# Optimization experiments

Hardware: AMD Instinct MI355X
Metric: run time of the kernel (lower is better)

The kernel has to match this reference:

```python
import jax, jax.numpy as jnp
import numpy as np


def _layernorm(x, g, b, eps=1e-6):
    mu = jnp.mean(x, -1, keepdims=True)
    var = jnp.var(x, -1, keepdims=True)
    return (x - mu) * jax.lax.rsqrt(var + eps) * g + b


def _rope_interleave(x, cos, sin):
    # de-interleave pairs (x0,x1),(x2,x3),... -> [evens | odds]  (matches
    # torch view(..., d//2, 2).transpose(-1,-2).reshape(..., d))
    x = jnp.concatenate([x[..., 0::2], x[..., 1::2]], axis=-1)
    d = x.shape[-1]
    x1, x2 = x[..., : d // 2], x[..., d // 2 :]
    rot = jnp.concatenate([-x2, x1], axis=-1)
    return x * cos + rot * sin


def setup_inputs() -> dict:
    key = jax.random.key(0)
    k = jax.random.split(key, 6)
    T, H, D, R, HID, QLR, K = 2048, 32, 128, 64, 4096, 1536, 256
    hidden_states = jax.random.normal(k[0], (1, T, HID), jnp.float32)
    q_latent = jax.random.normal(k[1], (1, T, QLR), jnp.float32)
    wq_b = jax.random.normal(k[2], (QLR, H * D), jnp.float32) * 0.02
    wk = jax.random.normal(k[3], (HID, D), jnp.float32) * 0.02
    w_proj = jax.random.normal(k[4], (HID, H), jnp.float32) * 0.02
    k_gamma = jnp.ones((D,), jnp.float32)
    k_beta = jnp.zeros((D,), jnp.float32)
    # real rotary cos/sin tables for the 64-dim rope slice
    pos = jnp.arange(T, dtype=jnp.float32)
    inv_freq = 1.0 / (10000.0 ** (jnp.arange(0, R, 2, dtype=jnp.float32) / R))
    freqs = jnp.outer(pos, inv_freq)
    emb = jnp.concatenate([freqs, freqs], axis=-1)  # [T, R]
    cos, sin = jnp.cos(emb), jnp.sin(emb)
    ks = jnp.zeros((T,), jnp.int32)
    ke = jnp.arange(1, T + 1, dtype=jnp.int32)  # causal: keys [0, t]
    return dict(hidden_states=hidden_states, q_latent=q_latent, ks=ks, ke=ke,
                cos=cos, sin=sin, wq_b=wq_b, wk=wk, k_gamma=k_gamma,
                k_beta=k_beta, w_proj=w_proj, index_topk=K)


def reference(hidden_states, q_latent, ks, ke, cos, sin, wq_b, wk,
              k_gamma, k_beta, w_proj, index_topk):
    T = hidden_states.shape[1]
    H = w_proj.shape[1]
    D = wk.shape[1]
    R = cos.shape[-1]
    weight_scale = (D ** -0.5) * (H ** -0.5)

    q = (q_latent[0] @ wq_b).reshape(T, H, D)              # [T,H,D]
    k = _layernorm(hidden_states[0] @ wk, k_gamma, k_beta)  # [T,D]
    w = hidden_states[0] @ w_proj                           # [T,H]

    q_pe = _rope_interleave(q[..., :R], cos[:, None, :], sin[:, None, :])
    k_pe = _rope_interleave(k[..., :R], cos, sin)
    q = jnp.concatenate([q_pe, q[..., R:]], axis=-1)
    k = jnp.concatenate([k_pe, k[..., R:]], axis=-1)

    # lightning-indexer score: I[t,s] = sum_h w[t,h] * relu(q[t,h] . k[s])
    scores = jnp.einsum('thd,sd->ths', q, k)                # [T,H,S]
    scores = jnp.einsum('ths,th->ts', jax.nn.relu(scores), w) * weight_scale

    j = jnp.arange(T)
    mask = (j[None, :] >= ks[:, None]) & (j[None, :] < ke[:, None])
    scores = jnp.where(mask, scores, -1e30)
    values, idx = jax.lax.top_k(scores, index_topk)
    return idx.reshape(1, T, 1, index_topk), values
```

## Files before the change

### kernel.cpp

```cpp
#include <hip/hip_runtime.h>
#include <cstdint>

typedef unsigned short u16;
typedef unsigned int   u32;
typedef unsigned long long u64;

typedef short bf16x8 __attribute__((ext_vector_type(8)));
typedef float f32x4  __attribute__((ext_vector_type(4)));
typedef u16   u16x8  __attribute__((ext_vector_type(8)));

__device__ __forceinline__ u16 f2b(float f){
  u32 u = __float_as_uint(f);
  u += 0x7FFFu + ((u >> 16) & 1u);
  return (u16)(u >> 16);
}
__device__ __forceinline__ float b2f(u16 h){ return __uint_as_float(((u32)h) << 16); }
__device__ __forceinline__ u32 fkey(float f){
  u32 u = __float_as_uint(f);
  return u ^ ((u & 0x80000000u) ? 0xFFFFFFFFu : 0x80000000u);
}
__device__ __forceinline__ float unkey(u32 k){
  u32 u = (k & 0x80000000u) ? (k ^ 0x80000000u) : ~k;
  return __uint_as_float(u);
}
__device__ __forceinline__ void gload16(const void* g, void* l){
  __builtin_amdgcn_global_load_lds(
      reinterpret_cast<const __attribute__((address_space(1))) char*>(reinterpret_cast<uintptr_t>(g)),
      reinterpret_cast<__attribute__((address_space(3))) char*>(reinterpret_cast<uintptr_t>(l)),
      16, 0, 0);
}

__global__ __launch_bounds__(256) void k_init(const int* __restrict__ ke, int* __restrict__ list){
  __shared__ int km[64];
  int tid = threadIdx.x;
  if (tid < 64){
    int m = 0;
    for (int j = 0; j < 32; j++) m = max(m, ke[tid * 32 + j]);
    km[tid] = m;
  }
  __syncthreads();
  if (tid < 8){
    int x = tid, n = 0;
    for (int j0 = 0; j0 < 8; j0++){
      int tb = j0 * 8 + x;
      int kmax = km[tb];
      for (int sb = 0; sb < 16; sb++){
        if (sb * 128 < kmax){
          list[n * 8 + x] = tb * 32 + sb * 2 + 0; n++;
          list[n * 8 + x] = tb * 32 + sb * 2 + 1; n++;
        }
      }
    }
    for (; n < 256; n++) list[n * 8 + x] = -1;
  }
}

__global__ __launch_bounds__(256) void k_cvt(const float* __restrict__ in, u16* __restrict__ out, int n8){
  int i = blockIdx.x * 256 + threadIdx.x;
  if (i >= n8) return;
  const float4* p = (const float4*)in + (size_t)i * 2;
  float4 a = p[0], b = p[1];
  u16x8 v;
  v[0]=f2b(a.x); v[1]=f2b(a.y); v[2]=f2b(a.z); v[3]=f2b(a.w);
  v[4]=f2b(b.x); v[5]=f2b(b.y); v[6]=f2b(b.z); v[7]=f2b(b.w);
  *((u16x8*)out + i) = v;
}

__global__ __launch_bounds__(256) void k_tcvt(const float* __restrict__ in, u16* __restrict__ out, int R, int C){
  __shared__ float tile[32][33];
  int c0 = blockIdx.x * 32, r0 = blockIdx.y * 32;
  int tx = threadIdx.x & 31, ty = threadIdx.x >> 5;
  for (int i = 0; i < 4; i++){
    int r = ty * 4 + i;
    tile[r][tx] = in[(size_t)(r0 + r) * C + c0 + tx];
  }
  __syncthreads();
  for (int i = 0; i < 4; i++){
    int c = ty * 4 + i;
    out[(size_t)(c0 + c) * R + r0 + tx] = f2b(tile[tx][c]);
  }
}

__global__ __launch_bounds__(256) void k_wct(const float* __restrict__ wk, const float* __restrict__ wp, u16* __restrict__ out){
  __shared__ float tile[32][33];
  int c0 = blockIdx.x * 32, i0 = blockIdx.y * 32;
  int tx = threadIdx.x & 31, ty = threadIdx.x >> 5;
  for (int j = 0; j < 4; j++){
    int i = i0 + ty * 4 + j;
    int c = c0 + tx;
    float v = 0.f;
    if (c < 128) v = wk[(size_t)i * 128 + c];
    else if (c < 160) v = wp[(size_t)i * 32 + (c - 128)];
    tile[ty * 4 + j][tx] = v;
  }
  __syncthreads();
  for (int j = 0; j < 4; j++){
    int c = c0 + ty * 4 + j;
    out[(size_t)c * 4096 + i0 + tx] = f2b(tile[tx][ty * 4 + j]);
  }
}

__global__ __launch_bounds__(256) void k_gemm_kw(const float* __restrict__ A, const u16* __restrict__ B, float* __restrict__ Cp){
  const int Kd = 4096, NC = 192;
  __shared__ float As[128 * 64];
  __shared__ u16 Bs[64 * 64];
  int lin = blockIdx.x;
  int xcd = lin & 7, idx = lin >> 3;
  int nb = idx % 3, pz = idx / 3;
  int p = xcd + 8 * pz;
  int m0 = (p & 15) * 128;
  int kt0 = (p >> 4) * 512;
  int n0 = nb * 64;
  float* C = Cp + (size_t)(p >> 4) * 2048 * NC;
  int tid = threadIdx.x, lane = tid & 63, wid = tid >> 6;
  int wm = wid * 32;
  f32x4 acc[2][4] = {};
  for (int kt = kt0; kt < kt0 + 512; kt += 64){
    for (int c = tid; c < 2048; c += 256){
      int row = c >> 4, slot = (c & 15) ^ (row & 7);
      gload16(A + (size_t)(m0 + row) * Kd + kt + slot * 4, (float*)As + (size_t)c * 4);
    }
    for (int c = tid; c < 512; c += 256){
      int row = c >> 3, slot = (c & 7) ^ (row & 7);
      gload16(B + (size_t)(n0 + row) * Kd + kt + slot * 8, (u16*)Bs + (size_t)c * 8);
    }
    __syncthreads();
    for (int kk = 0; kk < 2; kk++){
      bf16x8 af[2], bfr[4];
      for (int i = 0; i < 2; i++){
        int row = wm + i * 16 + (lane & 15);
        int c0 = kk * 8 + (lane >> 4) * 2;
        f32x4 lo = *(const f32x4*)&As[row * 64 + ((c0)     ^ (row & 7)) * 4];
        f32x4 hi = *(const f32x4*)&As[row * 64 + ((c0 + 1) ^ (row & 7)) * 4];
        bf16x8 t;
        t[0]=(short)f2b(lo[0]); t[1]=(short)f2b(lo[1]); t[2]=(short)f2b(lo[2]); t[3]=(short)f2b(lo[3]);
        t[4]=(short)f2b(hi[0]); t[5]=(short)f2b(hi[1]); t[6]=(short)f2b(hi[2]); t[7]=(short)f2b(hi[3]);
        af[i] = t;
      }
      for (int j = 0; j < 4; j++){
        int row = j * 16 + (lane & 15);
        int slot = (kk * 4 + (lane >> 4)) ^ (row & 7);
        bfr[j] = *(const bf16x8*)&Bs[row * 64 + slot * 8];
      }
      for (int i = 0; i < 2; i++)
        for (int j = 0; j < 4; j++)
          acc[i][j] = __builtin_amdgcn_mfma_f32_16x16x32_bf16(af[i], bfr[j], acc[i][j], 0, 0, 0);
    }
    __syncthreads();
  }
  for (int i = 0; i < 2; i++)
    for (int j = 0; j < 4; j++){
      int row = m0 + wm + i * 16 + ((lane >> 4) * 4);
      int col = n0 + j * 16 + (lane & 15);
      for (int r = 0; r < 4; r++)
        C[(size_t)(row + r) * NC + col] = acc[i][j][r];
    }
}

__global__ __launch_bounds__(256) void k_lnrope(const float* __restrict__ kwp, const float* __restrict__ gamma,
                                                const float* __restrict__ beta, const float* __restrict__ cosp,
                                                const float* __restrict__ sinp, u16* __restrict__ krot,
                                                float* __restrict__ wfin){
  const size_t ZS = (size_t)2048 * 192;
  int row = blockIdx.x * 4 + (threadIdx.x >> 6);
  int lane = threadIdx.x & 63;
  const float* x = kwp + (size_t)row * 192;
  float2 v = {0.f, 0.f};
  for (int z = 0; z < 8; z++){
    float2 p = *(const float2*)&x[z * ZS + lane * 2];
    v.x += p.x; v.y += p.y;
  }
  float s = v.x + v.y, ss = v.x * v.x + v.y * v.y;
  for (int o = 32; o; o >>= 1){ s += __shfl_xor(s, o); ss += __shfl_xor(ss, o); }
  float mu = s * (1.f / 128.f);
  float var = ss * (1.f / 128.f) - mu * mu;
  float rs = rsqrtf(var + 1e-6f);
  float y0 = (v.x - mu) * rs * gamma[lane * 2]     + beta[lane * 2];
  float y1 = (v.y - mu) * rs * gamma[lane * 2 + 1] + beta[lane * 2 + 1];
  u16* out = krot + (size_t)row * 128;
  if (lane < 32){
    float c = cosp[(size_t)row * 64 + lane], sn = sinp[(size_t)row * 64 + lane];
    out[lane]      = f2b(y0 * c - y1 * sn);
    out[lane + 32] = f2b(y1 * c + y0 * sn);
    float wsum = 0.f;
    for (int z = 0; z < 8; z++) wsum += x[z * ZS + 128 + lane];
    wfin[(size_t)row * 32 + lane] = wsum;
  } else {
    out[lane * 2]     = f2b(y0);
    out[lane * 2 + 1] = f2b(y1);
  }
}

__global__ __launch_bounds__(256) void k_gemm_q(const u16* __restrict__ A, const u16* __restrict__ B,
                                                const float* __restrict__ cosp, const float* __restrict__ sinp,
                                                u16* __restrict__ C){
  const int N = 4096, Kd = 1536;
  __shared__ u16 As[128 * 64];
  __shared__ u16 Bs[128 * 64];
  int linb = blockIdx.x;
  int xcd = linb & 7, loc = linb >> 3;
  int n0 = (xcd * 4 + (loc >> 4)) * 128;
  int m0 = (loc & 15) * 128;
  int tid = threadIdx.x, lane = tid & 63, wid = tid >> 6;
  int wm = (wid >> 1) * 64, wn = (wid & 1) * 64;
  f32x4 acc[4][4] = {};
  for (int kt = 0; kt < Kd; kt += 64){
    for (int c = tid; c < 1024; c += 256){
      int row = c >> 3, slot = (c & 7) ^ (row & 7);
      gload16(A + (size_t)(m0 + row) * Kd + kt + slot * 8, (u16*)As + (size_t)c * 8);
      gload16(B + (size_t)(n0 + row) * Kd + kt + slot * 8, (u16*)Bs + (size_t)c * 8);
    }
    __syncthreads();
    for (int kk = 0; kk < 2; kk++){
      bf16x8 af[4], bfr[4];
      for (int i = 0; i < 4; i++){
        int rowa = wm + i * 16 + (lane & 15);
        int rowb = wn + i * 16 + (lane & 15);
        int sa = (kk * 4 + (lane >> 4)) ^ (rowa & 7);
        int sbx = (kk * 4 + (lane >> 4)) ^ (rowb & 7);
        af[i]  = *(const bf16x8*)&As[rowa * 64 + sa * 8];
        bfr[i] = *(const bf16x8*)&Bs[rowb * 64 + sbx * 8];
      }
      for (int i = 0; i < 4; i++)
        for (int j = 0; j < 4; j++)
          acc[i][j] = __builtin_amdgcn_mfma_f32_16x16x32_bf16(af[i], bfr[j], acc[i][j], 0, 0, 0);
    }
    __syncthreads();
  }
  if (wn == 0){
    int l = lane & 15;
    int base = lane & 48;
    int sl = base + ((2 * l) & 15);
    for (int i = 0; i < 4; i++){
      int rowb = m0 + wm + i * 16 + ((lane >> 4) * 4);
      f32x4 ne[4];
      for (int j = 0; j < 4; j++){
        int jj = j & 1;
        for (int r = 0; r < 4; r++){
          float eA = __shfl(acc[i][2 * jj][r],     sl);
          float eB = __shfl(acc[i][2 * jj + 1][r], sl);
          float oA = __shfl(acc[i][2 * jj][r],     sl + 1);
          float oB = __shfl(acc[i][2 * jj + 1][r], sl + 1);
          float e = (l >= 8) ? eB : eA;
          float o = (l >= 8) ? oB : oA;
          int row = rowb + r;
          int d = j * 16 + l;
          float c = cosp[(size_t)row * 64 + d];
          float s = sinp[(size_t)row * 64 + d];
          ne[j][r] = (j < 2) ? (e * c - o * s) : (o * c + e * s);
        }
      }
      for (int j = 0; j < 4; j++) acc[i][j] = ne[j];
    }
  }
  for (int i = 0; i < 4; i++)
    for (int j = 0; j < 4; j++){
      int row = m0 + wm + i * 16 + ((lane >> 4) * 4);
      int col = n0 + wn + j * 16 + (lane & 15);
      for (int r = 0; r < 4; r++)
        C[(size_t)(row + r) * N + col] = f2b(acc[i][j][r]);
    }
}

__global__ __launch_bounds__(256, 4) void k_scores(const u16* __restrict__ q, const u16* __restrict__ krot,
                                                   const float* __restrict__ wfin, const int* __restrict__ list,
                                                   float* __restrict__ S0, float* __restrict__ S1){
  __shared__ u16 Bs[128 * 128];
  __shared__ float Ws[16][32];
  int e = list[blockIdx.x];
  if (e < 0) return;
  int tb = e >> 5, sb = (e >> 1) & 15, hgrp = e & 1;
  int t0 = tb * 32, s0 = sb * 128;
  int tid = threadIdx.x, lane = tid & 63, wid = tid >> 6;
  int wr = wid >> 1, wc = wid & 1;

  for (int c = tid; c < 2048; c += 256){
    int row = c >> 4, slot = (c & 15) ^ (row & 7);
    gload16(krot + (size_t)(s0 + row) * 128 + slot * 8, (u16*)Bs + (size_t)c * 8);
  }
  for (int i = tid; i < 512; i += 256){
    int h = i >> 5, r = i & 31;
    Ws[h][r] = wfin[(size_t)(t0 + r) * 32 + hgrp * 16 + h];
  }
  __syncthreads();

  bf16x8 bfr[4][4];
  for (int j = 0; j < 4; j++)
    for (int kc = 0; kc < 4; kc++){
      int row = wc * 64 + j * 16 + (lane & 15);
      int slot = (kc * 4 + (lane >> 4)) ^ (row & 7);
      bfr[j][kc] = *(const bf16x8*)&Bs[row * 128 + slot * 8];
    }

  f32x4 acc[4] = {};
  const u16* qbase = q + ((size_t)t0 + wr * 16 + (lane & 15)) * 4096 + (size_t)hgrp * 16 * 128 + (lane >> 4) * 8;
  int rbase = wr * 16 + ((lane >> 4) * 4);
  for (int h = 0; h < 16; h++){
    bf16x8 af[4];
    for (int kc = 0; kc < 4; kc++)
      af[kc] = *(const bf16x8*)&qbase[h * 128 + kc * 32];
    f32x4 ah[4] = {};
    for (int kc = 0; kc < 4; kc++)
      for (int j = 0; j < 4; j++)
        ah[j] = __builtin_amdgcn_mfma_f32_16x16x32_bf16(af[kc], bfr[j][kc], ah[j], 0, 0, 0);
    for (int r = 0; r < 4; r++){
      float wv = Ws[h][rbase + r];
      for (int j = 0; j < 4; j++)
        acc[j][r] += fmaxf(ah[j][r], 0.f) * wv;
    }
  }
  float* Sp = hgrp ? S1 : S0;
  for (int j = 0; j < 4; j++){
    int col = s0 + wc * 64 + j * 16 + (lane & 15);
    for (int r = 0; r < 4; r++)
      Sp[(size_t)(t0 + rbase + r) * 2048 + col] = acc[j][r];
  }
}

__global__ __launch_bounds__(256) void k_topk(const float* __restrict__ S0, const float* __restrict__ S1,
                                              const int* __restrict__ ktp, const int* __restrict__ ksv,
                                              const int* __restrict__ ke, float* __restrict__ out){
  int t = blockIdx.x;
  int T = gridDim.x;
  const float* r0 = S0 + (size_t)t * 2048;
  const float* r1 = S1 + (size_t)t * 2048;
  __shared__ u32 keys[2048];
  __shared__ u32 hist[256];
  __shared__ u32 ssum[256];
  __shared__ u32 sb, srem;
  __shared__ u32 wtot[8];
  __shared__ int selIdx[256];
  __shared__ u32 baseGt, baseTie;
  __shared__ u64 skey[256];
  int tid = threadIdx.x;
  int K = ktp[0]; if (K > 256) K = 256;
  int ket = ke[t]; if (ket < 0) ket = 0; if (ket > 2048) ket = 2048;
  int kst = ksv[t]; if (kst < 0) kst = 0;
  int limit = (ket + 255) & ~255;
  if (limit < 256) limit = 256;
  if (limit > 2048) limit = 2048;
  const u32 kneg = fkey(-1e30f);
  const float scale = 0.015625f;
  for (int i4 = tid; i4 < (limit >> 2); i4 += 256){
    int base = i4 * 4;
    float4 a = ((const float4*)r0)[i4];
    float4 b = ((const float4*)r1)[i4];
    float v0 = (a.x + b.x) * scale, v1 = (a.y + b.y) * scale;
    float v2 = (a.z + b.z) * scale, v3 = (a.w + b.w) * scale;
    keys[base + 0] = (base + 0 >= kst && base + 0 < ket) ? fkey(v0) : kneg;
    keys[base + 1] = (base + 1 >= kst && base + 1 < ket) ? fkey(v1) : kneg;
    keys[base + 2] = (base + 2 >= kst && base + 2 < ket) ? fkey(v2) : kneg;
    keys[base + 3] = (base + 3 >= kst && base + 3 < ket) ? fkey(v3) : kneg;
  }
  __syncthreads();
  if (limit > K){
    u32 prefix = 0, pmask = 0, rem = (u32)K;
    for (int p = 3; p >= 0; p--){
      int sh = p * 8;
      hist[tid] = 0;
      __syncthreads();
      for (int i = tid; i < limit; i += 256){
        u32 u = keys[i];
        if ((u & pmask) == prefix) atomicAdd(&hist[(u >> sh) & 255], 1u);
      }
      __syncthreads();
      ssum[tid] = hist[tid];
      __syncthreads();
      for (int off = 1; off < 256; off <<= 1){
        u32 add = (tid + off < 256) ? ssum[tid + off] : 0u;
        __syncthreads();
        ssum[tid] += add;
        __syncthreads();
      }
      u32 mine = ssum[tid];
      u32 above = (tid == 255) ? 0u : ssum[tid + 1];
      if (mine >= rem && above < rem){ sb = (u32)tid; srem = rem - above; }
      __syncthreads();
      prefix |= (sb << sh);
      pmask |= (255u << sh);
      rem = srem;
      __syncthreads();
    }
    u32 thr = prefix;
    int G = K - (int)rem;
    if (tid == 0){ baseGt = 0; baseTie = 0; }
    __syncthreads();
    int nch = limit >> 8;
    for (int ch = 0; ch < nch; ch++){
      int i = ch * 256 + tid;
      u32 u = keys[i];
      bool gt = (u > thr), tie = (u == thr);
      u64 bg = __ballot(gt), bt = __ballot(tie);
      int lane = tid & 63, w = tid >> 6;
      if (lane == 0){ wtot[w] = (u32)__popcll(bg); wtot[4 + w] = (u32)__popcll(bt); }
      __syncthreads();
      u32 og = baseGt, ot = baseTie;
      for (int ww = 0; ww < w; ww++){ og += wtot[ww]; ot += wtot[4 + ww]; }
      og += (u32)__popcll(bg & ((1ull << lane) - 1ull));
      ot += (u32)__popcll(bt & ((1ull << lane) - 1ull));
      if (gt) selIdx[og] = i;
      else if (tie && ot < rem) selIdx[G + ot] = i;
      __syncthreads();
      if (tid == 0){
        for (int ww = 0; ww < 4; ww++){ baseGt += wtot[ww]; baseTie += wtot[4 + ww]; }
      }
      __syncthreads();
    }
    if (tid < K){
      int si = selIdx[tid];
      u32 u = keys[si];
      skey[tid] = ((u64)(~u) << 32) | (u32)si;
    } else {
      skey[tid] = ~0ull;
    }
  } else {
    if (tid < K) skey[tid] = ((u64)(~keys[tid]) << 32) | (u32)tid;
    else skey[tid] = ~0ull;
  }
  __syncthreads();
  for (int size = 2; size <= 256; size <<= 1){
    for (int stride = size >> 1; stride > 0; stride >>= 1){
      int p = tid ^ stride;
      if (p > tid){
        bool up = ((tid & size) == 0);
        u64 a = skey[tid], b = skey[p];
        if ((a > b) == up){ skey[tid] = b; skey[p] = a; }
      }
      __syncthreads();
    }
  }
  if (tid < K){
    u64 sk = skey[tid];
    int idx = (int)(u32)(sk & 0xFFFFFFFFu);
    float val = unkey(~(u32)(sk >> 32));
    out[(size_t)t * K + tid] = (float)idx;
    out[(size_t)T * K + (size_t)t * K + tid] = val;
  }
}

extern "C" void kernel_launch(void* const* d_in, const int* in_sizes, int n_in,
                              void* d_out, int out_size, void* d_ws, size_t ws_size,
                              hipStream_t stream){
  const float* hs   = (const float*)d_in[0];
  const float* ql   = (const float*)d_in[1];
  const int*   ks   = (const int*)  d_in[2];
  const int*   ke   = (const int*)  d_in[3];
  const float* cosp = (const float*)d_in[4];
  const float* sinp = (const float*)d_in[5];
  const float* wqb  = (const float*)d_in[6];
  const float* wk   = (const float*)d_in[7];
  const float* kg   = (const float*)d_in[8];
  const float* kb   = (const float*)d_in[9];
  const float* wp   = (const float*)d_in[10];
  const int*   ktp  = (const int*)  d_in[11];

  char* w = (char*)d_ws;
  u16* qlb = (u16*)w;  w += (size_t)2048 * 1536 * 2;
  u16* wqT = (u16*)w;  w += (size_t)4096 * 1536 * 2;
  u16* wct = (u16*)w;  w += (size_t)192 * 4096 * 2;
  u16* qb  = (u16*)w;  w += (size_t)2048 * 4096 * 2;
  float* kwp = (float*)w; w += (size_t)8 * 2048 * 192 * 4;
  float* wfin = (float*)w; w += (size_t)2048 * 32 * 4;
  u16* krt = (u16*)w;  w += (size_t)2048 * 128 * 2;
  float* S0 = (float*)w; w += (size_t)2048 * 2048 * 4;
  int* list = (int*)w;  w += 2048 * 4;
  float* S1 = (float*)d_ws;

  hipLaunchKernelGGL(k_init, dim3(1), dim3(256), 0, stream, ke, list);
  hipLaunchKernelGGL(k_cvt, dim3(1536), dim3(256), 0, stream, ql, qlb, 393216);
  hipLaunchKernelGGL(k_tcvt, dim3(128, 48), dim3(256), 0, stream, wqb, wqT, 1536, 4096);
  hipLaunchKernelGGL(k_wct, dim3(6, 128), dim3(256), 0, stream, wk, wp, wct);
  hipLaunchKernelGGL(k_gemm_kw, dim3(384), dim3(256), 0, stream, hs, wct, kwp);
  hipLaunchKernelGGL(k_lnrope, dim3(512), dim3(256), 0, stream, kwp, kg, kb, cosp, sinp, krt, wfin);
  hipLaunchKernelGGL(k_gemm_q, dim3(512), dim3(256), 0, stream, qlb, wqT, cosp, sinp, qb);
  hipLaunchKernelGGL(k_scores, dim3(2048), dim3(256), 0, stream, qb, krt, wfin, list, S0, S1);
  hipLaunchKernelGGL(k_topk, dim3(2048), dim3(256), 0, stream, S0, S1, ktp, ks, ke, (float*)d_out);
}
```

Measured before the change: 158.3 us.

## Merge Q-projection and K/W-projection GEMMs into one horizontally fused launch

```diff
diff --git a/kernel.cpp b/kernel.cpp
--- a/kernel.cpp
+++ b/kernel.cpp
@@ -100,61 +100,134 @@
   }
 }
 
-__global__ __launch_bounds__(256) void k_gemm_kw(const float* __restrict__ A, const u16* __restrict__ B, float* __restrict__ Cp){
-  const int Kd = 4096, NC = 192;
-  __shared__ float As[128 * 64];
-  __shared__ u16 Bs[64 * 64];
-  int lin = blockIdx.x;
-  int xcd = lin & 7, idx = lin >> 3;
-  int nb = idx % 3, pz = idx / 3;
-  int p = xcd + 8 * pz;
-  int m0 = (p & 15) * 128;
-  int kt0 = (p >> 4) * 512;
-  int n0 = nb * 64;
-  float* C = Cp + (size_t)(p >> 4) * 2048 * NC;
+__global__ __launch_bounds__(256) void k_gemm_fused(const u16* __restrict__ Aq, const u16* __restrict__ Bq,
+                                                    const float* __restrict__ cosp, const float* __restrict__ sinp,
+                                                    u16* __restrict__ Cq,
+                                                    const float* __restrict__ Akw, const u16* __restrict__ Bkw,
+                                                    float* __restrict__ Cp){
+  __shared__ char smem[40960];
   int tid = threadIdx.x, lane = tid & 63, wid = tid >> 6;
-  int wm = wid * 32;
-  f32x4 acc[2][4] = {};
-  for (int kt = kt0; kt < kt0 + 512; kt += 64){
-    for (int c = tid; c < 2048; c += 256){
-      int row = c >> 4, slot = (c & 15) ^ (row & 7);
-      gload16(A + (size_t)(m0 + row) * Kd + kt + slot * 4, (float*)As + (size_t)c * 4);
-    }
-    for (int c = tid; c < 512; c += 256){
-      int row = c >> 3, slot = (c & 7) ^ (row & 7);
-      gload16(B + (size_t)(n0 + row) * Kd + kt + slot * 8, (u16*)Bs + (size_t)c * 8);
-    }
-    __syncthreads();
-    for (int kk = 0; kk < 2; kk++){
-      bf16x8 af[2], bfr[4];
-      for (int i = 0; i < 2; i++){
-        int row = wm + i * 16 + (lane & 15);
-        int c0 = kk * 8 + (lane >> 4) * 2;
-        f32x4 lo = *(const f32x4*)&As[row * 64 + ((c0)     ^ (row & 7)) * 4];
-        f32x4 hi = *(const f32x4*)&As[row * 64 + ((c0 + 1) ^ (row & 7)) * 4];
-        bf16x8 t;
-        t[0]=(short)f2b(lo[0]); t[1]=(short)f2b(lo[1]); t[2]=(short)f2b(lo[2]); t[3]=(short)f2b(lo[3]);
-        t[4]=(short)f2b(hi[0]); t[5]=(short)f2b(hi[1]); t[6]=(short)f2b(hi[2]); t[7]=(short)f2b(hi[3]);
-        af[i] = t;
-      }
+  if (blockIdx.x < 512){
+    const int N = 4096, Kd = 1536;
+    u16* As = (u16*)smem;
+    u16* Bs = (u16*)(smem + 16384);
+    int linb = blockIdx.x;
+    int xcd = linb & 7, loc = linb >> 3;
+    int n0 = (xcd * 4 + (loc >> 4)) * 128;
+    int m0 = (loc & 15) * 128;
+    int wm = (wid >> 1) * 64, wn = (wid & 1) * 64;
+    f32x4 acc[4][4] = {};
+    for (int kt = 0; kt < Kd; kt += 64){
+      for (int c = tid; c < 1024; c += 256){
+        int row = c >> 3, slot = (c & 7) ^ (row & 7);
+        gload16(Aq + (size_t)(m0 + row) * Kd + kt + slot * 8, As + (size_t)c * 8);
+        gload16(Bq + (size_t)(n0 + row) * Kd + kt + slot * 8, Bs + (size_t)c * 8);
+      }
+      __syncthreads();
+      for (int kk = 0; kk < 2; kk++){
+        bf16x8 af[4], bfr[4];
+        for (int i = 0; i < 4; i++){
+          int rowa = wm + i * 16 + (lane & 15);
+          int rowb = wn + i * 16 + (lane & 15);
+          int sa = (kk * 4 + (lane >> 4)) ^ (rowa & 7);
+          int sbx = (kk * 4 + (lane >> 4)) ^ (rowb & 7);
+          af[i]  = *(const bf16x8*)&As[rowa * 64 + sa * 8];
+          bfr[i] = *(const bf16x8*)&Bs[rowb * 64 + sbx * 8];
+        }
+        for (int i = 0; i < 4; i++)
+          for (int j = 0; j < 4; j++)
+            acc[i][j] = __builtin_amdgcn_mfma_f32_16x16x32_bf16(af[i], bfr[j], acc[i][j], 0, 0, 0);
+      }
+      __syncthreads();
+    }
+    if (wn == 0){
+      int l = lane & 15;
+      int base = lane & 48;
+      int sl = base + ((2 * l) & 15);
+      for (int i = 0; i < 4; i++){
+        int rowb = m0 + wm + i * 16 + ((lane >> 4) * 4);
+        f32x4 ne[4];
+        for (int j = 0; j < 4; j++){
+          int jj = j & 1;
+          for (int r = 0; r < 4; r++){
+            float eA = __shfl(acc[i][2 * jj][r],     sl);
+            float eB = __shfl(acc[i][2 * jj + 1][r], sl);
+            float oA = __shfl(acc[i][2 * jj][r],     sl + 1);
+            float oB = __shfl(acc[i][2 * jj + 1][r], sl + 1);
+            float e = (l >= 8) ? eB : eA;
+            float o = (l >= 8) ? oB : oA;
+            int row = rowb + r;
+            int d = j * 16 + l;
+            float c = cosp[(size_t)row * 64 + d];
+            float s = sinp[(size_t)row * 64 + d];
+            ne[j][r] = (j < 2) ? (e * c - o * s) : (o * c + e * s);
+          }
+        }
+        for (int j = 0; j < 4; j++) acc[i][j] = ne[j];
+      }
+    }
+    for (int i = 0; i < 4; i++)
       for (int j = 0; j < 4; j++){
-        int row = j * 16 + (lane & 15);
-        int slot = (kk * 4 + (lane >> 4)) ^ (row & 7);
-        bfr[j] = *(const bf16x8*)&Bs[row * 64 + slot * 8];
-      }
-      for (int i = 0; i < 2; i++)
-        for (int j = 0; j < 4; j++)
-          acc[i][j] = __builtin_amdgcn_mfma_f32_16x16x32_bf16(af[i], bfr[j], acc[i][j], 0, 0, 0);
-    }
-    __syncthreads();
-  }
-  for (int i = 0; i < 2; i++)
-    for (int j = 0; j < 4; j++){
-      int row = m0 + wm + i * 16 + ((lane >> 4) * 4);
-      int col = n0 + j * 16 + (lane & 15);
-      for (int r = 0; r < 4; r++)
-        C[(size_t)(row + r) * NC + col] = acc[i][j][r];
-    }
+        int row = m0 + wm + i * 16 + ((lane >> 4) * 4);
+        int col = n0 + wn + j * 16 + (lane & 15);
+        for (int r = 0; r < 4; r++)
+          Cq[(size_t)(row + r) * N + col] = f2b(acc[i][j][r]);
+      }
+  } else {
+    const int Kd = 4096, NC = 192;
+    float* As = (float*)smem;
+    u16* Bs = (u16*)(smem + 32768);
+    int lin = blockIdx.x - 512;
+    int xcd = lin & 7, idx = lin >> 3;
+    int nb = idx % 3, pz = idx / 3;
+    int p = xcd + 8 * pz;
+    int m0 = (p & 15) * 128;
+    int kt0 = (p >> 4) * 512;
+    int n0 = nb * 64;
+    float* C = Cp + (size_t)(p >> 4) * 2048 * NC;
+    int wm = wid * 32;
+    f32x4 acc[2][4] = {};
+    for (int kt = kt0; kt < kt0 + 512; kt += 64){
+      for (int c = tid; c < 2048; c += 256){
+        int row = c >> 4, slot = (c & 15) ^ (row & 7);
+        gload16(Akw + (size_t)(m0 + row) * Kd + kt + slot * 4, As + (size_t)c * 4);
+      }
+      for (int c = tid; c < 512; c += 256){
+        int row = c >> 3, slot = (c & 7) ^ (row & 7);
+        gload16(Bkw + (size_t)(n0 + row) * Kd + kt + slot * 8, Bs + (size_t)c * 8);
+      }
+      __syncthreads();
+      for (int kk = 0; kk < 2; kk++){
+        bf16x8 af[2], bfr[4];
+        for (int i = 0; i < 2; i++){
+          int row = wm + i * 16 + (lane & 15);
+          int c0 = kk * 8 + (lane >> 4) * 2;
+          f32x4 lo = *(const f32x4*)&As[row * 64 + ((c0)     ^ (row & 7)) * 4];
+          f32x4 hi = *(const f32x4*)&As[row * 64 + ((c0 + 1) ^ (row & 7)) * 4];
+          bf16x8 t;
+          t[0]=(short)f2b(lo[0]); t[1]=(short)f2b(lo[1]); t[2]=(short)f2b(lo[2]); t[3]=(short)f2b(lo[3]);
+          t[4]=(short)f2b(hi[0]); t[5]=(short)f2b(hi[1]); t[6]=(short)f2b(hi[2]); t[7]=(short)f2b(hi[3]);
+          af[i] = t;
+        }
+        for (int j = 0; j < 4; j++){
+          int row = j * 16 + (lane & 15);
+          int slot = (kk * 4 + (lane >> 4)) ^ (row & 7);
+          bfr[j] = *(const bf16x8*)&Bs[row * 64 + slot * 8];
+        }
+        for (int i = 0; i < 2; i++)
+          for (int j = 0; j < 4; j++)
+            acc[i][j] = __builtin_amdgcn_mfma_f32_16x16x32_bf16(af[i], bfr[j], acc[i][j], 0, 0, 0);
+      }
+      __syncthreads();
+    }
+    for (int i = 0; i < 2; i++)
+      for (int j = 0; j < 4; j++){
+        int row = m0 + wm + i * 16 + ((lane >> 4) * 4);
+        int col = n0 + j * 16 + (lane & 15);
+        for (int r = 0; r < 4; r++)
+          C[(size_t)(row + r) * NC + col] = acc[i][j][r];
+      }
+  }
 }
 
 __global__ __launch_bounds__(256) void k_lnrope(const float* __restrict__ kwp, const float* __restrict__ gamma,
@@ -189,77 +262,6 @@
     out[lane * 2]     = f2b(y0);
     out[lane * 2 + 1] = f2b(y1);
   }
-}
-
-__global__ __launch_bounds__(256) void k_gemm_q(const u16* __restrict__ A, const u16* __restrict__ B,
-                                                const float* __restrict__ cosp, const float* __restrict__ sinp,
-                                                u16* __restrict__ C){
-  const int N = 4096, Kd = 1536;
-  __shared__ u16 As[128 * 64];
-  __shared__ u16 Bs[128 * 64];
-  int linb = blockIdx.x;
-  int xcd = linb & 7, loc = linb >> 3;
-  int n0 = (xcd * 4 + (loc >> 4)) * 128;
-  int m0 = (loc & 15) * 128;
-  int tid = threadIdx.x, lane = tid & 63, wid = tid >> 6;
-  int wm = (wid >> 1) * 64, wn = (wid & 1) * 64;
-  f32x4 acc[4][4] = {};
-  for (int kt = 0; kt < Kd; kt += 64){
-    for (int c = tid; c < 1024; c += 256){
-      int row = c >> 3, slot = (c & 7) ^ (row & 7);
-      gload16(A + (size_t)(m0 + row) * Kd + kt + slot * 8, (u16*)As + (size_t)c * 8);
-      gload16(B + (size_t)(n0 + row) * Kd + kt + slot * 8, (u16*)Bs + (size_t)c * 8);
-    }
-    __syncthreads();
-    for (int kk = 0; kk < 2; kk++){
-      bf16x8 af[4], bfr[4];
-      for (int i = 0; i < 4; i++){
-        int rowa = wm + i * 16 + (lane & 15);
-        int rowb = wn + i * 16 + (lane & 15);
-        int sa = (kk * 4 + (lane >> 4)) ^ (rowa & 7);
-        int sbx = (kk * 4 + (lane >> 4)) ^ (rowb & 7);
-        af[i]  = *(const bf16x8*)&As[rowa * 64 + sa * 8];
-        bfr[i] = *(const bf16x8*)&Bs[rowb * 64 + sbx * 8];
-      }
-      for (int i = 0; i < 4; i++)
-        for (int j = 0; j < 4; j++)
-          acc[i][j] = __builtin_amdgcn_mfma_f32_16x16x32_bf16(af[i], bfr[j], acc[i][j], 0, 0, 0);
-    }
-    __syncthreads();
-  }
-  if (wn == 0){
-    int l = lane & 15;
-    int base = lane & 48;
-    int sl = base + ((2 * l) & 15);
-    for (int i = 0; i < 4; i++){
-      int rowb = m0 + wm + i * 16 + ((lane >> 4) * 4);
-      f32x4 ne[4];
-      for (int j = 0; j < 4; j++){
-        int jj = j & 1;
-        for (int r = 0; r < 4; r++){
-          float eA = __shfl(acc[i][2 * jj][r],     sl);
-          float eB = __shfl(acc[i][2 * jj + 1][r], sl);
-          float oA = __shfl(acc[i][2 * jj][r],     sl + 1);
-          float oB = __shfl(acc[i][2 * jj + 1][r], sl + 1);
-          float e = (l >= 8) ? eB : eA;
-          float o = (l >= 8) ? oB : oA;
-          int row = rowb + r;
-          int d = j * 16 + l;
-          float c = cosp[(size_t)row * 64 + d];
-          float s = sinp[(size_t)row * 64 + d];
-          ne[j][r] = (j < 2) ? (e * c - o * s) : (o * c + e * s);
-        }
-      }
-      for (int j = 0; j < 4; j++) acc[i][j] = ne[j];
-    }
-  }
-  for (int i = 0; i < 4; i++)
-    for (int j = 0; j < 4; j++){
-      int row = m0 + wm + i * 16 + ((lane >> 4) * 4);
-      int col = n0 + wn + j * 16 + (lane & 15);
-      for (int r = 0; r < 4; r++)
-        C[(size_t)(row + r) * N + col] = f2b(acc[i][j][r]);
-    }
 }
 
 __global__ __launch_bounds__(256, 4) void k_scores(const u16* __restrict__ q, const u16* __restrict__ krot,
@@ -470,9 +472,9 @@
   hipLaunchKernelGGL(k_cvt, dim3(1536), dim3(256), 0, stream, ql, qlb, 393216);
   hipLaunchKernelGGL(k_tcvt, dim3(128, 48), dim3(256), 0, stream, wqb, wqT, 1536, 4096);
   hipLaunchKernelGGL(k_wct, dim3(6, 128), dim3(256), 0, stream, wk, wp, wct);
-  hipLaunchKernelGGL(k_gemm_kw, dim3(384), dim3(256), 0, stream, hs, wct, kwp);
+  hipLaunchKernelGGL(k_gemm_fused, dim3(896), dim3(256), 0, stream,
+                     qlb, wqT, cosp, sinp, qb, hs, wct, kwp);
   hipLaunchKernelGGL(k_lnrope, dim3(512), dim3(256), 0, stream, kwp, kg, kb, cosp, sinp, krt, wfin);
-  hipLaunchKernelGGL(k_gemm_q, dim3(512), dim3(256), 0, stream, qlb, wqT, cosp, sinp, qb);
   hipLaunchKernelGGL(k_scores, dim3(2048), dim3(256), 0, stream, qb, krt, wfin, list, S0, S1);
   hipLaunchKernelGGL(k_topk, dim3(2048), dim3(256), 0, stream, S0, S1, ktp, ks, ke, (float*)d_out);
 }
```

Result: faster. 154.7 us (-2.3%).
